# Optimization experiments

Hardware: AMD Instinct MI355X
Metric: run time of the kernel (lower is better)

Reference implementation:

```python
import jax, jax.numpy as jnp
import numpy as np

EMB_DIM = 16

def _pos_enc_table(side_len, emb_dim):
    pos = np.arange(side_len)[:, None].astype(np.float64)
    j = np.arange(emb_dim)[None, :]
    enc = pos / np.power(10000.0, 2.0 * (j // 2) / emb_dim)
    enc[0, :] = 0.0
    enc[1:, 0::2] = np.sin(enc[1:, 0::2])
    enc[1:, 1::2] = np.cos(enc[1:, 1::2])
    return enc.astype(np.float32)  # [L, E]

def _pos_embeddings(side_len, emb_dim):
    t = _pos_enc_table(side_len, emb_dim)
    # original uses raw .view (row-major reshape), NOT a transpose
    x = np.tile(t.reshape(1, emb_dim, side_len, 1), (1, 1, 1, side_len))
    y = np.tile(t.reshape(1, emb_dim, 1, side_len), (1, 1, side_len, 1))
    return jnp.asarray(np.concatenate((x, y), axis=1))  # [1, 2E, L, L]

def setup_inputs() -> dict:
    key = jax.random.key(0)
    ks = jax.random.split(key, 7)
    B, C, L = 32, 224, 32
    Cin = C + 2 * EMB_DIM  # 256
    K = V = 256
    s = 0.02
    return {
        "x": jax.random.normal(ks[0], (B, C, L, L), dtype=jnp.float32),
        "wq": jax.random.normal(ks[1], (K, Cin), dtype=jnp.float32) * s,
        "bq": jax.random.normal(ks[2], (K,), dtype=jnp.float32) * s,
        "wk": jax.random.normal(ks[3], (K, Cin), dtype=jnp.float32) * s,
        "bk": jax.random.normal(ks[4], (K,), dtype=jnp.float32) * s,
        "wv": jax.random.normal(ks[5], (V, Cin), dtype=jnp.float32) * s,
        "bv": jax.random.normal(ks[6], (V,), dtype=jnp.float32) * s,
    }

def reference(x, wq, bq, wk, bk, wv, bv):
    B, C, H, W = x.shape
    S = H * W
    Kdim = wq.shape[0]
    Vdim = wv.shape[0]
    pe = _pos_embeddings(H, EMB_DIM).astype(x.dtype)  # [1, 2E, H, W]
    x0 = jnp.concatenate([x, jnp.broadcast_to(pe, (B, 2 * EMB_DIM, H, W))], axis=1)
    x0 = x0.reshape(B, C + 2 * EMB_DIM, S)  # [B, Cin, S]
    # 1x1 conv == channel matmul, then ReLU nonlin
    q = jax.nn.relu(jnp.einsum('kc,bcs->bks', wq, x0) + bq[None, :, None])
    k = jax.nn.relu(jnp.einsum('kc,bcs->bks', wk, x0) + bk[None, :, None])
    v = jax.nn.relu(jnp.einsum('vc,bcs->bvs', wv, x0) + bv[None, :, None])
    attn = jnp.einsum('bks,bkt->bst', q, k) / jnp.sqrt(jnp.asarray(Kdim, x.dtype))
    mask = jnp.tril(jnp.ones((S, S), dtype=x.dtype))  # causal incl. self
    attn = attn * mask + (1.0 - mask) * (-10000.0)
    attn = jax.nn.softmax(attn, axis=-1) * mask  # double masking as in source
    out1 = jnp.einsum('bst,bvt->bvs', attn, v)  # [B, V, S]
    # NOTE: source computes out1 + fc(out1) but then overwrites with out1.view(...)
    return out1.reshape(B, Vdim, H, W)
```

## Files before the change

kernel.cpp:

```cpp
#include <hip/hip_runtime.h>
#include <cstdint>

typedef float  f32x4  __attribute__((ext_vector_type(4)));
typedef short  short8 __attribute__((ext_vector_type(8)));
typedef _Float16 half4 __attribute__((ext_vector_type(4)));
typedef _Float16 half8 __attribute__((ext_vector_type(8)));

__device__ __forceinline__ unsigned short f2bf(float f) {
    unsigned u = __builtin_bit_cast(unsigned, f);
    u += 0x7FFFu + ((u >> 16) & 1u);
    return (unsigned short)(u >> 16);
}

__global__ void wconv_kernel(const float* __restrict__ wq,
                             const float* __restrict__ wk,
                             const float* __restrict__ wv,
                             unsigned short* __restrict__ Wb) {
    int p = blockIdx.x >> 8;
    int i = ((blockIdx.x & 255) << 8) + threadIdx.x;
    const float* src = (p == 0) ? wq : ((p == 1) ? wk : wv);
    Wb[(p << 16) + i] = f2bf(src[i]);
}

__global__ void build_x0_kernel(const float* __restrict__ x,
                                unsigned short* __restrict__ X0) {
    __shared__ float tile[32][33];
    int b  = blockIdx.z;
    int ct = blockIdx.y;
    int st = blockIdx.x;
    int tid = threadIdx.x;
    int lo = tid & 31, hi = tid >> 5;

    if (ct < 7) {
        #pragma unroll
        for (int r = 0; r < 4; ++r) {
            int c = hi + 8 * r;
            tile[c][lo] = x[((b * 224 + ct * 32 + c) << 10) + st * 32 + lo];
        }
        __syncthreads();
        #pragma unroll
        for (int r = 0; r < 4; ++r) {
            int s_loc = hi + 8 * r;
            X0[(((b << 10) + st * 32 + s_loc) << 8) + ct * 32 + lo] = f2bf(tile[lo][s_loc]);
        }
    } else {
        #pragma unroll
        for (int r = 0; r < 4; ++r) {
            int s_loc = hi + 8 * r;
            int s = st * 32 + s_loc;
            int h = s >> 5, w = s & 31;
            int ch = lo;
            int i = (ch < 16) ? (ch * 32 + h) : ((ch - 16) * 32 + w);
            int l = i >> 4, e = i & 15;
            float val = 0.f;
            if (l > 0) {
                float ang = (float)l * powf(10000.f, -(float)(e >> 1) * 0.125f);
                val = (e & 1) ? cosf(ang) : sinf(ang);
            }
            X0[(((b << 10) + s) << 8) + 224 + ch] = f2bf(val);
        }
    }
}

__global__ __launch_bounds__(256) void proj_kernel(
        const unsigned short* __restrict__ X0,
        const unsigned short* __restrict__ Wb,
        const float* __restrict__ bq, const float* __restrict__ bk,
        const float* __restrict__ bv,
        unsigned short* __restrict__ Q, unsigned short* __restrict__ K,
        _Float16* __restrict__ V) {
    __shared__ __align__(16) char Xlds[32768];
    __shared__ __align__(16) char Wlds[32768];

    int pb = blockIdx.z; int proj = pb >> 5; int b = pb & 31;
    int tid = threadIdx.x; int w = tid >> 6; int l = tid & 63;
    int g = l >> 4, c = l & 15;
    int wr = w >> 1, wc = w & 1;
    int sb = blockIdx.x * 64;
    int o0 = blockIdx.y * 64;
    const unsigned short* Wp = Wb + (proj << 16);
    const float* bias = (proj == 0) ? bq : ((proj == 1) ? bk : bv);

    const unsigned short* Xg = &X0[((b << 10) + sb) << 8];
    #pragma unroll
    for (int p = 0; p < 8; ++p) {
        int ch = p * 256 + tid;
        int row = ch >> 5;
        int cl = (ch & 31) ^ (row & 7);
        __builtin_amdgcn_global_load_lds(
            (const unsigned int*)&Xg[(row << 8) + cl * 8],
            (unsigned int*)(Xlds + ((p << 8) + (w << 6)) * 16), 16, 0, 0);
    }
    const unsigned short* Wg = &Wp[o0 << 8];
    #pragma unroll
    for (int p = 0; p < 8; ++p) {
        int ch = p * 256 + tid;
        int row = ch >> 5;
        int cl = (ch & 31) ^ (row & 7);
        __builtin_amdgcn_global_load_lds(
            (const unsigned int*)&Wg[(row << 8) + cl * 8],
            (unsigned int*)(Wlds + ((p << 8) + (w << 6)) * 16), 16, 0, 0);
    }
    asm volatile("s_waitcnt vmcnt(0)\n\ts_barrier" ::: "memory");

    f32x4 acc[2][2];
    #pragma unroll
    for (int i = 0; i < 2; ++i)
        #pragma unroll
        for (int j = 0; j < 2; ++j) acc[i][j] = (f32x4){0.f, 0.f, 0.f, 0.f};

    const char* abase0 = &Xlds[(wr * 32 + c) * 512];
    const char* abase1 = &Xlds[(wr * 32 + 16 + c) * 512];
    const char* bbase0 = &Wlds[(wc * 32 + c) * 512];
    const char* bbase1 = &Wlds[(wc * 32 + 16 + c) * 512];

    __builtin_amdgcn_s_setprio(1);
    #pragma unroll
    for (int kk = 0; kk < 8; ++kk) {
        int co = ((kk * 4 + g) ^ (c & 7)) << 4;
        short8 a0 = *(const short8*)&abase0[co];
        short8 a1 = *(const short8*)&abase1[co];
        short8 b0 = *(const short8*)&bbase0[co];
        short8 b1 = *(const short8*)&bbase1[co];
        acc[0][0] = __builtin_amdgcn_mfma_f32_16x16x32_bf16(a0, b0, acc[0][0], 0, 0, 0);
        acc[0][1] = __builtin_amdgcn_mfma_f32_16x16x32_bf16(a0, b1, acc[0][1], 0, 0, 0);
        acc[1][0] = __builtin_amdgcn_mfma_f32_16x16x32_bf16(a1, b0, acc[1][0], 0, 0, 0);
        acc[1][1] = __builtin_amdgcn_mfma_f32_16x16x32_bf16(a1, b1, acc[1][1], 0, 0, 0);
    }
    __builtin_amdgcn_s_setprio(0);

    #pragma unroll
    for (int j = 0; j < 2; ++j) {
        int o = o0 + wc * 32 + j * 16 + c;
        float bb = bias[o];
        #pragma unroll
        for (int i = 0; i < 2; ++i) {
            int sgb = sb + wr * 32 + i * 16;
            if (proj < 2) {
                unsigned short* dst = (proj == 0) ? Q : K;
                #pragma unroll
                for (int r = 0; r < 4; ++r) {
                    float v = fmaxf(acc[i][j][r] + bb, 0.f);
                    int s = sgb + 4 * g + r;
                    dst[(((b << 10) + s) << 8) + o] = f2bf(v);
                }
            } else {
                half4 hv;
                #pragma unroll
                for (int r = 0; r < 4; ++r)
                    hv[r] = (_Float16)fmaxf(acc[i][j][r] + bb, 0.f);
                int hi = (sgb >> 4) & 1;
                *(half4*)&V[(((b << 8) + o) << 10) + ((sgb >> 5) << 5)
                            + (g << 3) + (hi << 2)] = hv;
            }
        }
    }
}

__global__ __launch_bounds__(256, 2) void attn_kernel(
        const unsigned short* __restrict__ Q,
        const unsigned short* __restrict__ K,
        const _Float16* __restrict__ V,
        float* __restrict__ out) {
    __shared__ __align__(16) char Klds[2][16384];
    __shared__ __align__(16) char Vlds[2][16384];

    int bid = blockIdx.x;
    int xcd  = bid & 7;
    int qv   = (bid >> 3) & 7;
    int bhi  = (bid >> 6) & 3;
    int hf   = bid >> 8;
    int b  = (bhi << 3) | xcd;
    int qt = hf ? qv : (15 - qv);

    int tid = threadIdx.x; int w = tid >> 6; int l = tid & 63;
    int g = l >> 4, c = l & 15;
    int s0 = (qt << 6) + (w << 4);

    short8 qf[8];
    #pragma unroll
    for (int kk = 0; kk < 8; ++kk)
        qf[kk] = *(const short8*)&Q[(((b << 10) + s0 + c) << 8) + kk * 32 + g * 8];

    float m = -1e30f, lsum = 0.f;
    f32x4 acc[16];
    #pragma unroll
    for (int i = 0; i < 16; ++i) acc[i] = (f32x4){0.f, 0.f, 0.f, 0.f};

    const unsigned short* Kb_ = &K[(size_t)b << 18];
    const _Float16*       Vb_ = &V[(size_t)b << 18];

    int nt = 2 * qt + 2;
    int dt = 2 * qt + (w >> 1);

    auto stage = [&](int t, int bufi) {
        int t0 = t << 5;
        #pragma unroll
        for (int j = 0; j < 4; ++j) {
            int ch = (j << 8) + tid;
            int trow = ch >> 5;
            int cl = (ch & 31) ^ (trow & 7);
            __builtin_amdgcn_global_load_lds(
                (const unsigned int*)&Kb_[((t0 + trow) << 8) + cl * 8],
                (unsigned int*)(Klds[bufi] + ((j << 8) + (w << 6)) * 16), 16, 0, 0);
        }
        #pragma unroll
        for (int j = 0; j < 4; ++j) {
            int ch = (j << 8) + tid;
            int v = ch >> 2;
            int gq = (ch & 3) ^ ((v >> 1) & 3);
            __builtin_amdgcn_global_load_lds(
                (const unsigned int*)&Vb_[(v << 10) + (t << 5) + gq * 8],
                (unsigned int*)(Vlds[bufi] + ((j << 8) + (w << 6)) * 16), 16, 0, 0);
        }
    };

    stage(0, 0);

    for (int t = 0; t < nt; ++t) {
        asm volatile("s_waitcnt vmcnt(0)\n\ts_barrier" ::: "memory");
        if (t + 1 < nt) stage(t + 1, (t + 1) & 1);
        if (t > dt) continue;

        const char* Kl = Klds[t & 1];
        const char* Vl = Vlds[t & 1];
        half8 vread[16];
        #pragma unroll
        for (int vt = 0; vt < 16; ++vt) {
            int pos = (vt << 6) + (c << 2) + (g ^ ((c >> 1) & 3));
            vread[vt] = *(const half8*)&Vl[pos << 4];
        }
        #pragma unroll
        for (int sub = 0; sub < 2; ++sub) {
            bool dmask = (t == dt) && (sub == (w & 1));
            if ((t == dt) && !(w & 1) && sub == 1) break;
            int toff = sub << 4;
            f32x4 sc0 = {0.f,0.f,0.f,0.f}, sc1 = {0.f,0.f,0.f,0.f};
            const char* kbase = &Kl[(toff + c) * 512];
            __builtin_amdgcn_s_setprio(1);
            #pragma unroll
            for (int kk = 0; kk < 8; kk += 2) {
                short8 a0 = *(const short8*)&kbase[(((kk * 4 + g)       ^ (c & 7)) << 4)];
                short8 a1 = *(const short8*)&kbase[((((kk + 1) * 4 + g) ^ (c & 7)) << 4)];
                sc0 = __builtin_amdgcn_mfma_f32_16x16x32_bf16(a0, qf[kk], sc0, 0, 0, 0);
                sc1 = __builtin_amdgcn_mfma_f32_16x16x32_bf16(a1, qf[kk + 1], sc1, 0, 0, 0);
            }
            __builtin_amdgcn_s_setprio(0);
            float sv[4];
            #pragma unroll
            for (int r = 0; r < 4; ++r) sv[r] = (sc0[r] + sc1[r]) * 0.0625f;
            if (dmask) {
                #pragma unroll
                for (int r = 0; r < 4; ++r)
                    if (4 * g + r > c) sv[r] = -1e30f;
            }
            float tm = fmaxf(fmaxf(sv[0], sv[1]), fmaxf(sv[2], sv[3]));
            if (!__all((int)(tm <= m + 8.f))) {
                float tr = fmaxf(tm, __shfl_xor(tm, 16));
                tr = fmaxf(tr, __shfl_xor(tr, 32));
                float mnew = fmaxf(m, tr);
                float alpha = __expf(m - mnew);
                m = mnew;
                lsum *= alpha;
                #pragma unroll
                for (int i = 0; i < 16; ++i) acc[i] *= alpha;
            }
            float p[4];
            #pragma unroll
            for (int r = 0; r < 4; ++r) { p[r] = __expf(sv[r] - m); lsum += p[r]; }
            half4 pb;
            #pragma unroll
            for (int r = 0; r < 4; ++r) pb[r] = (_Float16)p[r];
            __builtin_amdgcn_s_setprio(1);
            #pragma unroll
            for (int vt = 0; vt < 16; ++vt) {
                half4 vf;
                #pragma unroll
                for (int jj = 0; jj < 4; ++jj) vf[jj] = vread[vt][sub * 4 + jj];
                acc[vt] = __builtin_amdgcn_mfma_f32_16x16x16f16(vf, pb, acc[vt], 0, 0, 0);
            }
            __builtin_amdgcn_s_setprio(0);
        }
    }

    lsum += __shfl_xor(lsum, 16);
    lsum += __shfl_xor(lsum, 32);
    float rl = 1.f / lsum;
    #pragma unroll
    for (int vt = 0; vt < 16; ++vt) {
        #pragma unroll
        for (int r = 0; r < 4; ++r)
            out[(((b << 8) + vt * 16 + 4 * g + r) << 10) + s0 + c] = acc[vt][r] * rl;
    }
}

extern "C" void kernel_launch(void* const* d_in, const int* in_sizes, int n_in,
                              void* d_out, int out_size, void* d_ws, size_t ws_size,
                              hipStream_t stream) {
    const float* x  = (const float*)d_in[0];
    const float* wq = (const float*)d_in[1];
    const float* bq = (const float*)d_in[2];
    const float* wk = (const float*)d_in[3];
    const float* bk = (const float*)d_in[4];
    const float* wv = (const float*)d_in[5];
    const float* bv = (const float*)d_in[6];
    float* out = (float*)d_out;

    char* ws = (char*)d_ws;
    unsigned short* Wb = (unsigned short*)ws;
    unsigned short* X0 = (unsigned short*)(ws + 393216);
    unsigned short* Qb = (unsigned short*)(ws + 393216 + 16777216);
    unsigned short* Kb = (unsigned short*)(ws + 393216 + 2 * 16777216);
    _Float16*       Vb = (_Float16*)     (ws + 393216 + 3 * 16777216);

    wconv_kernel<<<768, 256, 0, stream>>>(wq, wk, wv, Wb);
    build_x0_kernel<<<dim3(32, 8, 32), 256, 0, stream>>>(x, X0);
    proj_kernel<<<dim3(16, 4, 96), 256, 0, stream>>>(X0, Wb, bq, bk, bv, Qb, Kb, Vb);
    attn_kernel<<<512, 256, 0, stream>>>(Qb, Kb, Vb, out);
}
```

Before: 111.9 us.

## Fuse x0 construction into projection kernel, reuse X tile across all projections

Removes the separate build_x0 kernel and its bf16 X0 workspace round trip. Each block now transposes and converts its 64-position slice of x (plus positional encodings) directly into LDS, holds the A fragments in registers, and loops over all three projections and four output tiles, streaming weight tiles into LDS. This cuts global traffic and one launch, but leaves only 512 blocks that each do serial work with a barrier per weight tile and no overlap of weight loads with compute. Register pressure from the held fragments also rises.

```diff
diff --git a/kernel.cpp b/kernel.cpp
--- a/kernel.cpp
+++ b/kernel.cpp
@@ -22,48 +22,8 @@
     Wb[(p << 16) + i] = f2bf(src[i]);
 }
 
-__global__ void build_x0_kernel(const float* __restrict__ x,
-                                unsigned short* __restrict__ X0) {
-    __shared__ float tile[32][33];
-    int b  = blockIdx.z;
-    int ct = blockIdx.y;
-    int st = blockIdx.x;
-    int tid = threadIdx.x;
-    int lo = tid & 31, hi = tid >> 5;
-
-    if (ct < 7) {
-        #pragma unroll
-        for (int r = 0; r < 4; ++r) {
-            int c = hi + 8 * r;
-            tile[c][lo] = x[((b * 224 + ct * 32 + c) << 10) + st * 32 + lo];
-        }
-        __syncthreads();
-        #pragma unroll
-        for (int r = 0; r < 4; ++r) {
-            int s_loc = hi + 8 * r;
-            X0[(((b << 10) + st * 32 + s_loc) << 8) + ct * 32 + lo] = f2bf(tile[lo][s_loc]);
-        }
-    } else {
-        #pragma unroll
-        for (int r = 0; r < 4; ++r) {
-            int s_loc = hi + 8 * r;
-            int s = st * 32 + s_loc;
-            int h = s >> 5, w = s & 31;
-            int ch = lo;
-            int i = (ch < 16) ? (ch * 32 + h) : ((ch - 16) * 32 + w);
-            int l = i >> 4, e = i & 15;
-            float val = 0.f;
-            if (l > 0) {
-                float ang = (float)l * powf(10000.f, -(float)(e >> 1) * 0.125f);
-                val = (e & 1) ? cosf(ang) : sinf(ang);
-            }
-            X0[(((b << 10) + s) << 8) + 224 + ch] = f2bf(val);
-        }
-    }
-}
-
-__global__ __launch_bounds__(256) void proj_kernel(
-        const unsigned short* __restrict__ X0,
+__global__ __launch_bounds__(256, 2) void fproj_kernel(
+        const float* __restrict__ x,
         const unsigned short* __restrict__ Wb,
         const float* __restrict__ bq, const float* __restrict__ bk,
         const float* __restrict__ bv,
@@ -71,88 +31,137 @@
         _Float16* __restrict__ V) {
     __shared__ __align__(16) char Xlds[32768];
     __shared__ __align__(16) char Wlds[32768];
-
-    int pb = blockIdx.z; int proj = pb >> 5; int b = pb & 31;
+    float* Tt = (float*)Wlds;
+
+    int st = blockIdx.x;
+    int b  = blockIdx.y;
+    int sb = st << 6;
     int tid = threadIdx.x; int w = tid >> 6; int l = tid & 63;
     int g = l >> 4, c = l & 15;
     int wr = w >> 1, wc = w & 1;
-    int sb = blockIdx.x * 64;
-    int o0 = blockIdx.y * 64;
-    const unsigned short* Wp = Wb + (proj << 16);
-    const float* bias = (proj == 0) ? bq : ((proj == 1) ? bk : bv);
-
-    const unsigned short* Xg = &X0[((b << 10) + sb) << 8];
+
+    #pragma unroll 1
+    for (int sc = 0; sc < 2; ++sc) {
+        if (sc) __syncthreads();
+        #pragma unroll
+        for (int r = 0; r < 28; ++r) {
+            int idx = r * 256 + tid;
+            int cc = idx >> 5, lo = idx & 31;
+            Tt[cc * 33 + lo] = x[((b * 224 + cc) << 10) + sb + (sc << 5) + lo];
+        }
+        __syncthreads();
+        #pragma unroll
+        for (int r = 0; r < 4; ++r) {
+            int idx = r * 256 + tid;
+            if (idx < 896) {
+                int cc16 = idx >> 5;
+                int sl = idx & 31;
+                int s = (sc << 5) + sl;
+                short8 v8;
+                #pragma unroll
+                for (int j = 0; j < 8; ++j)
+                    v8[j] = (short)f2bf(Tt[(cc16 * 8 + j) * 33 + sl]);
+                *(short8*)&Xlds[(s << 9) + ((cc16 ^ (s & 7)) << 4)] = v8;
+            }
+        }
+        if (tid < 128) {
+            int sl = tid >> 2;
+            int cc16 = 28 + (tid & 3);
+            int s = (sc << 5) + sl;
+            int sg = sb + s;
+            int h = sg >> 5, ww = sg & 31;
+            short8 v8;
+            #pragma unroll
+            for (int j = 0; j < 8; ++j) {
+                int ch = (cc16 - 28) * 8 + j;
+                int i = (ch < 16) ? (ch * 32 + h) : ((ch - 16) * 32 + ww);
+                int ll = i >> 4, e = i & 15;
+                float val = 0.f;
+                if (ll > 0) {
+                    float ang = (float)ll * powf(10000.f, -(float)(e >> 1) * 0.125f);
+                    val = (e & 1) ? cosf(ang) : sinf(ang);
+                }
+                v8[j] = (short)f2bf(val);
+            }
+            *(short8*)&Xlds[(s << 9) + ((cc16 ^ (s & 7)) << 4)] = v8;
+        }
+    }
+    __syncthreads();
+
+    short8 af[2][8];
     #pragma unroll
-    for (int p = 0; p < 8; ++p) {
-        int ch = p * 256 + tid;
-        int row = ch >> 5;
-        int cl = (ch & 31) ^ (row & 7);
-        __builtin_amdgcn_global_load_lds(
-            (const unsigned int*)&Xg[(row << 8) + cl * 8],
-            (unsigned int*)(Xlds + ((p << 8) + (w << 6)) * 16), 16, 0, 0);
-    }
-    const unsigned short* Wg = &Wp[o0 << 8];
-    #pragma unroll
-    for (int p = 0; p < 8; ++p) {
-        int ch = p * 256 + tid;
-        int row = ch >> 5;
-        int cl = (ch & 31) ^ (row & 7);
-        __builtin_amdgcn_global_load_lds(
-            (const unsigned int*)&Wg[(row << 8) + cl * 8],
-            (unsigned int*)(Wlds + ((p << 8) + (w << 6)) * 16), 16, 0, 0);
-    }
-    asm volatile("s_waitcnt vmcnt(0)\n\ts_barrier" ::: "memory");
-
-    f32x4 acc[2][2];
-    #pragma unroll
-    for (int i = 0; i < 2; ++i)
-        #pragma unroll
-        for (int j = 0; j < 2; ++j) acc[i][j] = (f32x4){0.f, 0.f, 0.f, 0.f};
-
-    const char* abase0 = &Xlds[(wr * 32 + c) * 512];
-    const char* abase1 = &Xlds[(wr * 32 + 16 + c) * 512];
-    const char* bbase0 = &Wlds[(wc * 32 + c) * 512];
-    const char* bbase1 = &Wlds[(wc * 32 + 16 + c) * 512];
-
-    __builtin_amdgcn_s_setprio(1);
-    #pragma unroll
-    for (int kk = 0; kk < 8; ++kk) {
-        int co = ((kk * 4 + g) ^ (c & 7)) << 4;
-        short8 a0 = *(const short8*)&abase0[co];
-        short8 a1 = *(const short8*)&abase1[co];
-        short8 b0 = *(const short8*)&bbase0[co];
-        short8 b1 = *(const short8*)&bbase1[co];
-        acc[0][0] = __builtin_amdgcn_mfma_f32_16x16x32_bf16(a0, b0, acc[0][0], 0, 0, 0);
-        acc[0][1] = __builtin_amdgcn_mfma_f32_16x16x32_bf16(a0, b1, acc[0][1], 0, 0, 0);
-        acc[1][0] = __builtin_amdgcn_mfma_f32_16x16x32_bf16(a1, b0, acc[1][0], 0, 0, 0);
-        acc[1][1] = __builtin_amdgcn_mfma_f32_16x16x32_bf16(a1, b1, acc[1][1], 0, 0, 0);
-    }
-    __builtin_amdgcn_s_setprio(0);
-
-    #pragma unroll
-    for (int j = 0; j < 2; ++j) {
-        int o = o0 + wc * 32 + j * 16 + c;
-        float bb = bias[o];
-        #pragma unroll
-        for (int i = 0; i < 2; ++i) {
-            int sgb = sb + wr * 32 + i * 16;
-            if (proj < 2) {
-                unsigned short* dst = (proj == 0) ? Q : K;
-                #pragma unroll
-                for (int r = 0; r < 4; ++r) {
-                    float v = fmaxf(acc[i][j][r] + bb, 0.f);
-                    int s = sgb + 4 * g + r;
-                    dst[(((b << 10) + s) << 8) + o] = f2bf(v);
+    for (int i = 0; i < 2; ++i) {
+        const char* ab = &Xlds[(wr * 32 + i * 16 + c) << 9];
+        #pragma unroll
+        for (int kk = 0; kk < 8; ++kk)
+            af[i][kk] = *(const short8*)&ab[((kk * 4 + g) ^ (c & 7)) << 4];
+    }
+
+    #pragma unroll 1
+    for (int pj = 0; pj < 3; ++pj) {
+        const float* bias = (pj == 0) ? bq : ((pj == 1) ? bk : bv);
+        #pragma unroll 1
+        for (int ot = 0; ot < 4; ++ot) {
+            const unsigned short* Wg = Wb + (pj << 16) + (ot << 14);
+            #pragma unroll
+            for (int p = 0; p < 8; ++p) {
+                int ch = p * 256 + tid;
+                int row = ch >> 5;
+                int cl = (ch & 31) ^ (row & 7);
+                __builtin_amdgcn_global_load_lds(
+                    (const unsigned int*)&Wg[(row << 8) + cl * 8],
+                    (unsigned int*)(Wlds + ((p << 8) + (w << 6)) * 16), 16, 0, 0);
+            }
+            asm volatile("s_waitcnt vmcnt(0)\n\ts_barrier" ::: "memory");
+
+            f32x4 acc[2][2];
+            #pragma unroll
+            for (int i = 0; i < 2; ++i)
+                #pragma unroll
+                for (int j = 0; j < 2; ++j) acc[i][j] = (f32x4){0.f, 0.f, 0.f, 0.f};
+
+            const char* bb0 = &Wlds[(wc * 32 + c) << 9];
+            const char* bb1 = &Wlds[(wc * 32 + 16 + c) << 9];
+            __builtin_amdgcn_s_setprio(1);
+            #pragma unroll
+            for (int kk = 0; kk < 8; ++kk) {
+                int co = ((kk * 4 + g) ^ (c & 7)) << 4;
+                short8 b0 = *(const short8*)&bb0[co];
+                short8 b1 = *(const short8*)&bb1[co];
+                acc[0][0] = __builtin_amdgcn_mfma_f32_16x16x32_bf16(af[0][kk], b0, acc[0][0], 0, 0, 0);
+                acc[0][1] = __builtin_amdgcn_mfma_f32_16x16x32_bf16(af[0][kk], b1, acc[0][1], 0, 0, 0);
+                acc[1][0] = __builtin_amdgcn_mfma_f32_16x16x32_bf16(af[1][kk], b0, acc[1][0], 0, 0, 0);
+                acc[1][1] = __builtin_amdgcn_mfma_f32_16x16x32_bf16(af[1][kk], b1, acc[1][1], 0, 0, 0);
+            }
+            __builtin_amdgcn_s_setprio(0);
+
+            #pragma unroll
+            for (int j = 0; j < 2; ++j) {
+                int o = (ot << 6) + wc * 32 + j * 16 + c;
+                float bbv = bias[o];
+                #pragma unroll
+                for (int i = 0; i < 2; ++i) {
+                    int sgb = sb + wr * 32 + i * 16;
+                    if (pj < 2) {
+                        unsigned short* dst = (pj == 0) ? Q : K;
+                        #pragma unroll
+                        for (int r = 0; r < 4; ++r) {
+                            float v = fmaxf(acc[i][j][r] + bbv, 0.f);
+                            int s = sgb + 4 * g + r;
+                            dst[(((b << 10) + s) << 8) + o] = f2bf(v);
+                        }
+                    } else {
+                        half4 hv;
+                        #pragma unroll
+                        for (int r = 0; r < 4; ++r)
+                            hv[r] = (_Float16)fmaxf(acc[i][j][r] + bbv, 0.f);
+                        int hi = (sgb >> 4) & 1;
+                        *(half4*)&V[(((b << 8) + o) << 10) + ((sgb >> 5) << 5)
+                                    + (g << 3) + (hi << 2)] = hv;
+                    }
                 }
-            } else {
-                half4 hv;
-                #pragma unroll
-                for (int r = 0; r < 4; ++r)
-                    hv[r] = (_Float16)fmaxf(acc[i][j][r] + bb, 0.f);
-                int hi = (sgb >> 4) & 1;
-                *(half4*)&V[(((b << 8) + o) << 10) + ((sgb >> 5) << 5)
-                            + (g << 3) + (hi << 2)] = hv;
-            }
+            }
+            __syncthreads();
         }
     }
 }
@@ -308,13 +317,11 @@
 
     char* ws = (char*)d_ws;
     unsigned short* Wb = (unsigned short*)ws;
-    unsigned short* X0 = (unsigned short*)(ws + 393216);
-    unsigned short* Qb = (unsigned short*)(ws + 393216 + 16777216);
-    unsigned short* Kb = (unsigned short*)(ws + 393216 + 2 * 16777216);
-    _Float16*       Vb = (_Float16*)     (ws + 393216 + 3 * 16777216);
+    unsigned short* Qb = (unsigned short*)(ws + 393216);
+    unsigned short* Kb = (unsigned short*)(ws + 393216 + 16777216);
+    _Float16*       Vb = (_Float16*)     (ws + 393216 + 2 * 16777216);
 
     wconv_kernel<<<768, 256, 0, stream>>>(wq, wk, wv, Wb);
-    build_x0_kernel<<<dim3(32, 8, 32), 256, 0, stream>>>(x, X0);
-    proj_kernel<<<dim3(16, 4, 96), 256, 0, stream>>>(X0, Wb, bq, bk, bv, Qb, Kb, Vb);
+    fproj_kernel<<<dim3(16, 32), 256, 0, stream>>>(x, Wb, bq, bk, bv, Qb, Kb, Vb);
     attn_kernel<<<512, 256, 0, stream>>>(Qb, Kb, Vb, out);
 }
```

After: 103.4 us. 7.7% less time.
